# Kernel optimization log

Hardware: AMD Instinct MI355X
Metric: run time of the kernel (lower is better)

Reference implementation:

```python
import jax, jax.numpy as jnp
import numpy as np
from jax import lax

N = 14
K = 512
NUM_CLASSES = 10
TAO = 0.5 / (N * N)
BETA = 2.0


def make_t_p(n=N, tao=TAO, beta=BETA):
    # t_p[i, j, a, b] = tao * max(1 - beta * (|a-i| + |b-j|) / n, -1)
    idx = jnp.arange(n, dtype=jnp.float32)
    d = (jnp.abs(idx[:, None, None, None] - idx[None, None, :, None])
         + jnp.abs(idx[None, :, None, None] - idx[None, None, None, :]))
    return (tao * jnp.maximum(1.0 - beta * d / n, -1.0)).astype(jnp.float32)


def masked_output(x, t_p):
    # Vectorized equivalent of computeMaskedOutput: global spatial argmax per
    # (batch, channel) selects a template, then masked = relu(x * template).
    B, H, W, C = x.shape
    flat_idx = jnp.argmax(x.reshape(B, H * W, C), axis=1)      # [B, C]
    pi, pj = flat_idx // W, flat_idx % W
    tpl = t_p[pi, pj]                                          # [B, C, H, W]
    tpl = jnp.transpose(tpl, (0, 2, 3, 1))                     # [B, H, W, C]
    masked = jax.nn.relu(x * tpl)
    return masked, x, tpl


def compute_loss(x, pos_templates, act_sums, cls_sums, gt):
    # Fused segment-sum form of the original nested python loops.
    classes = jnp.zeros(NUM_CLASSES, x.dtype).at[gt].add(1.0)  # bincount
    cls_new = cls_sums + classes
    means = jnp.mean(x, axis=(1, 2))                           # [B, C]
    onehot = jax.nn.one_hot(gt, NUM_CLASSES, dtype=x.dtype)    # [B, 10]
    act_new = act_sums + means.T @ onehot                      # [C, 10]
    # divide_no_nan
    fm = jnp.where(cls_new[None, :] == 0, 0.0,
                   act_new / jnp.where(cls_new[None, :] == 0, 1.0, cls_new[None, :]))
    fclass = jnp.argmax(fm, axis=1)                            # [C]
    match = fclass[None, :] == gt[:, None]                     # [B, C]
    pt = jax.nn.relu(pos_templates)
    # relu(t_n) == 0 since t_n is strictly negative
    loss = jnp.where(match[:, None, None, :], pt, 0.0)
    return loss, act_new, cls_new


def forward(inputs, gt, conv_w, conv_b, dense_w, dense_b,
            activation_sums_1, activation_sums_2, class_sums_1, class_sums_2):
    t_p = make_t_p()
    raw_map = inputs  # base_model treated as identity on its feature map
    x1, X1_relu, pos_t1 = masked_output(raw_map, t_p)
    x3 = jax.nn.relu(lax.conv_general_dilated(
        x1, conv_w, window_strides=(1, 1), padding='SAME',
        dimension_numbers=('NHWC', 'HWIO', 'NHWC')) + conv_b)
    x2, X2_relu, pos_t2 = masked_output(x3, t_p)
    pooled = lax.reduce_window(x2, -jnp.inf, lax.max,
                               (1, 2, 2, 1), (1, 2, 2, 1), 'VALID')
    flat = pooled.reshape(pooled.shape[0], -1)
    probs = jax.nn.softmax(flat @ dense_w + dense_b, axis=-1)
    loss1, as1, cs1 = compute_loss(x1, pos_t1, activation_sums_1, class_sums_1, gt)
    loss2, as2, cs2 = compute_loss(x2, pos_t2, activation_sums_2, class_sums_2, gt)
    return probs, x1, x2, loss1, loss2, raw_map, pos_t1


def setup_inputs() -> dict:
    key = jax.random.key(0)
    ks = jax.random.split(key, 4)
    B = 128
    inputs = jax.random.uniform(ks[0], (B, N, N, K), dtype=jnp.float32)
    gt = jax.random.randint(ks[1], (B,), 0, NUM_CLASSES)
    conv_w = jax.random.normal(ks[2], (3, 3, K, K), dtype=jnp.float32) * 0.02
    conv_b = jnp.zeros((K,), jnp.float32)
    D = (N // 2) * (N // 2) * K  # 25088
    dense_w = jax.random.normal(ks[3], (D, NUM_CLASSES), dtype=jnp.float32) * 0.02
    dense_b = jnp.zeros((NUM_CLASSES,), jnp.float32)
    return {
        'inputs': inputs, 'gt': gt,
        'conv_w': conv_w, 'conv_b': conv_b,
        'dense_w': dense_w, 'dense_b': dense_b,
        'activation_sums_1': jnp.zeros((K, NUM_CLASSES), jnp.float32),
        'activation_sums_2': jnp.zeros((K, NUM_CLASSES), jnp.float32),
        'class_sums_1': jnp.zeros((NUM_CLASSES,), jnp.float32),
        'class_sums_2': jnp.zeros((NUM_CLASSES,), jnp.float32),
    }


def reference(inputs, gt, conv_w, conv_b, dense_w, dense_b,
              activation_sums_1, activation_sums_2, class_sums_1, class_sums_2):
    return forward(inputs, gt, conv_w, conv_b, dense_w, dense_b,
                   activation_sums_1, activation_sums_2,
                   class_sums_1, class_sums_2)
```

## Files before the change

kernel.cpp:

```cpp
#include <hip/hip_runtime.h>
#include <hip/hip_bf16.h>
#include <stdint.h>

#define TAO_F (0.5f/196.0f)

typedef short s16x8 __attribute__((ext_vector_type(8)));
typedef float f32x4 __attribute__((ext_vector_type(4)));
typedef __attribute__((address_space(1))) const unsigned int u32_g;
typedef __attribute__((address_space(3))) unsigned int u32_l;

__device__ __forceinline__ void async_ld16(const void* g, void* l) {
  __builtin_amdgcn_global_load_lds((u32_g*)g, (u32_l*)l, 16, 0, 0);
}

__global__ void k_prep_w(const float* __restrict__ w, __hip_bfloat16* __restrict__ wT) {
  __shared__ float tile[64][65];
  int bid = blockIdx.x;
  int r = bid / 64; int rem = bid - r * 64;
  int cib = (rem >> 3) * 64, cob = (rem & 7) * 64;
  int tid = threadIdx.x;
  int col = tid & 63, rw = tid >> 6;
#pragma unroll
  for (int p = 0; p < 16; ++p) {
    int row = p * 4 + rw;
    tile[row][col] = w[(size_t)(r * 512 + cib + row) * 512 + cob + col];
  }
  __syncthreads();
#pragma unroll
  for (int p = 0; p < 16; ++p) {
    int row = p * 4 + rw;
    wT[(size_t)(r * 512 + cob + row) * 512 + cib + col] = __float2bfloat16(tile[col][row]);
  }
}

__global__ void k_fuse1(const float* __restrict__ in, const int* __restrict__ gt,
                        float* __restrict__ o_raw, float* __restrict__ o_x1,
                        float* __restrict__ o_t1, __hip_bfloat16* __restrict__ x1p,
                        float* __restrict__ act1, int* __restrict__ idx1) {
  int t = blockIdx.x * 256 + threadIdx.x;
  int b = t >> 9, c = t & 511;
  const float* ip = in + (size_t)b * 196 * 512 + c;
  float* rp = o_raw + (size_t)b * 196 * 512 + c;
  float best = -1e30f; int bi = 0;
  for (int s = 0; s < 196; ++s) {
    float v = ip[(size_t)s * 512];
    rp[(size_t)s * 512] = v;
    if (v > best) { best = v; bi = s; }
  }
  idx1[t] = bi;
  int pi = bi / 14, pj = bi - pi * 14;
  float* ox = o_x1 + (size_t)b * 196 * 512 + c;
  float* ot = o_t1 + (size_t)b * 196 * 512 + c;
  __hip_bfloat16* xp = x1p + ((size_t)(b * 16 + 1) * 16 + 1) * 512 + c;
  float sum = 0.f;
  for (int i = 0; i < 14; ++i) {
    int di = (i > pi) ? (i - pi) : (pi - i);
    for (int j = 0; j < 14; ++j) {
      int d = di + ((j > pj) ? (j - pj) : (pj - j));
      float tpl = TAO_F * fmaxf(1.0f - (float)d / 7.0f, -1.0f);
      float x = ip[(size_t)(i * 14 + j) * 512];
      float m = fmaxf(x * tpl, 0.0f);
      ox[(size_t)(i * 14 + j) * 512] = m;
      ot[(size_t)(i * 14 + j) * 512] = tpl;
      xp[(size_t)(i * 16 + j) * 512] = __float2bfloat16(m);
      sum += m;
    }
  }
  atomicAdd(&act1[c * 10 + gt[b]], sum * (1.0f / 196.0f));
}

__global__ __launch_bounds__(256, 3) void k_gemm(const __hip_bfloat16* __restrict__ x1p,
                                                 const __hip_bfloat16* __restrict__ wT,
                                                 const float* __restrict__ conv_b,
                                                 float* __restrict__ x3) {
  int bid = blockIdx.x;
  int nt4 = bid & 3; int mt196 = bid >> 2;
  int m0 = mt196 * 128, co0 = nt4 * 128;
  int tid = threadIdx.x;
  int lane = tid & 63;

  __shared__ short As[128 * 64];
  __shared__ short Bs[128 * 64];

  int srow = tid >> 3;
  int sslot = tid & 7;
  int sx = ((sslot ^ (srow & 7)) * 8);

  int baseA[4];
#pragma unroll
  for (int p = 0; p < 4; ++p) {
    int m = m0 + p * 32 + srow;
    int b = m / 196; int s = m - b * 196; int i = s / 14; int j = s - i * 14;
    baseA[p] = ((b * 16 + i + 1) * 16 + (j + 1)) * 512;
  }
  int baseB[4];
#pragma unroll
  for (int p = 0; p < 4; ++p) baseB[p] = (co0 + p * 32 + srow) * 512;

  f32x4 acc[4][4] = {};

  int m_off = (tid >> 7) * 64;
  int n_off = ((tid >> 6) & 1) * 64;
  int q = lane >> 4;
  int l16 = lane & 15;

  for (int r = 0; r < 9; ++r) {
    int offr = ((r / 3) * 16 + (r % 3) - 17) * 512;
    int wbase = r * 512 * 512;
    for (int cb = 0; cb < 8; ++cb) {
      int ko = cb * 64;
      __syncthreads();
#pragma unroll
      for (int p = 0; p < 4; ++p) {
        async_ld16(x1p + (baseA[p] + offr + ko + sx),
                   &As[(p * 32 + srow) * 64 + sslot * 8]);
        async_ld16(wT + (wbase + baseB[p] + ko + sx),
                   &Bs[(p * 32 + srow) * 64 + sslot * 8]);
      }
      __syncthreads();
#pragma unroll
      for (int kk = 0; kk < 2; ++kk) {
        s16x8 af[4], bf[4];
#pragma unroll
        for (int tt = 0; tt < 4; ++tt) {
          int rowa = m_off + tt * 16 + l16;
          int sa = (kk * 4 + q) ^ (rowa & 7);
          af[tt] = *(const s16x8*)&As[rowa * 64 + sa * 8];
          int rowb = n_off + tt * 16 + l16;
          int sb = (kk * 4 + q) ^ (rowb & 7);
          bf[tt] = *(const s16x8*)&Bs[rowb * 64 + sb * 8];
        }
#pragma unroll
        for (int mt = 0; mt < 4; ++mt)
#pragma unroll
          for (int nt = 0; nt < 4; ++nt)
            acc[mt][nt] = __builtin_amdgcn_mfma_f32_16x16x32_bf16(af[mt], bf[nt], acc[mt][nt], 0, 0, 0);
      }
    }
  }
#pragma unroll
  for (int nt = 0; nt < 4; ++nt) {
    int col = co0 + n_off + nt * 16 + l16;
    float bias = conv_b[col];
#pragma unroll
    for (int mt = 0; mt < 4; ++mt) {
      int mrow = m0 + m_off + mt * 16 + q * 4;
#pragma unroll
      for (int rg = 0; rg < 4; ++rg) {
        float v = acc[mt][nt][rg] + bias;
        x3[(size_t)(mrow + rg) * 512 + col] = fmaxf(v, 0.0f);
      }
    }
  }
}

__global__ void k_fuse2(const float* __restrict__ x3, const int* __restrict__ gt,
                        const float* __restrict__ dw, float* __restrict__ o_x2,
                        float* __restrict__ act2, float* __restrict__ logits,
                        int* __restrict__ idx2) {
  int t = blockIdx.x * 256 + threadIdx.x;
  int b = t >> 9, c = t & 511;
  const float* ip = x3 + (size_t)b * 196 * 512 + c;
  float best = -1e30f; int bi = 0;
  for (int s = 0; s < 196; ++s) {
    float v = ip[(size_t)s * 512];
    if (v > best) { best = v; bi = s; }
  }
  idx2[t] = bi;
  int pi = bi / 14, pj = bi - pi * 14;
  float* ox = o_x2 + (size_t)b * 196 * 512 + c;
  float sum = 0.f;
  float a[10] = {0.f,0.f,0.f,0.f,0.f,0.f,0.f,0.f,0.f,0.f};
  for (int ii = 0; ii < 7; ++ii) {
    float rv[2][14];
#pragma unroll
    for (int r2 = 0; r2 < 2; ++r2) {
      int i = 2 * ii + r2;
      int di = (i > pi) ? (i - pi) : (pi - i);
#pragma unroll
      for (int j = 0; j < 14; ++j) {
        int d = di + ((j > pj) ? (j - pj) : (pj - j));
        float tpl = TAO_F * fmaxf(1.0f - (float)d / 7.0f, -1.0f);
        float x = ip[(size_t)(i * 14 + j) * 512];
        float m = fmaxf(x * tpl, 0.0f);
        ox[(size_t)(i * 14 + j) * 512] = m;
        sum += m;
        rv[r2][j] = m;
      }
    }
#pragma unroll
    for (int jj = 0; jj < 7; ++jj) {
      float pm = fmaxf(fmaxf(rv[0][2 * jj], rv[0][2 * jj + 1]),
                       fmaxf(rv[1][2 * jj], rv[1][2 * jj + 1]));
      const float* wr = dw + ((size_t)((ii * 7 + jj) * 512 + c)) * 10;
#pragma unroll
      for (int t2 = 0; t2 < 10; ++t2) a[t2] += pm * wr[t2];
    }
  }
  atomicAdd(&act2[c * 10 + gt[b]], sum * (1.0f / 196.0f));
  __shared__ float red[10];
  if (threadIdx.x < 10) red[threadIdx.x] = 0.f;
  __syncthreads();
  int lane = threadIdx.x & 63;
#pragma unroll
  for (int t2 = 0; t2 < 10; ++t2) {
    float v = a[t2];
    for (int off = 32; off > 0; off >>= 1) v += __shfl_down(v, off);
    if (lane == 0) atomicAdd(&red[t2], v);
  }
  __syncthreads();
  if (threadIdx.x < 10) atomicAdd(&logits[b * 10 + threadIdx.x], red[threadIdx.x]);
}

__global__ void k_stats(const float* __restrict__ act1, const float* __restrict__ act2,
                        const float* __restrict__ as1, const float* __restrict__ as2,
                        const float* __restrict__ cs1, const float* __restrict__ cs2,
                        const int* __restrict__ gt, const float* __restrict__ logits,
                        const float* __restrict__ db, int* __restrict__ fc1,
                        int* __restrict__ fc2, float* __restrict__ o_probs) {
  __shared__ int scnt[10];
  int tid = threadIdx.x;
  if (tid < 10) scnt[tid] = 0;
  __syncthreads();
  if (tid < 128) atomicAdd(&scnt[gt[tid]], 1);
  __syncthreads();
  int c = tid;
  float best1 = -1e30f, best2 = -1e30f; int b1 = 0, b2 = 0;
#pragma unroll
  for (int g = 0; g < 10; ++g) {
    float cnt = (float)scnt[g];
    float cn1 = cs1[g] + cnt;
    float cn2 = cs2[g] + cnt;
    float a1 = act1[c * 10 + g] + as1[c * 10 + g];
    float a2 = act2[c * 10 + g] + as2[c * 10 + g];
    float f1 = (cn1 == 0.f) ? 0.f : a1 / cn1;
    float f2 = (cn2 == 0.f) ? 0.f : a2 / cn2;
    if (f1 > best1) { best1 = f1; b1 = g; }
    if (f2 > best2) { best2 = f2; b2 = g; }
  }
  fc1[c] = b1; fc2[c] = b2;
  if (tid < 128) {
    float l[10]; float m = -1e30f;
#pragma unroll
    for (int t2 = 0; t2 < 10; ++t2) { l[t2] = logits[tid * 10 + t2] + db[t2]; m = fmaxf(m, l[t2]); }
    float s = 0.f;
#pragma unroll
    for (int t2 = 0; t2 < 10; ++t2) { l[t2] = expf(l[t2] - m); s += l[t2]; }
    float inv = 1.0f / s;
#pragma unroll
    for (int t2 = 0; t2 < 10; ++t2) o_probs[tid * 10 + t2] = l[t2] * inv;
  }
}

__global__ void k_loss(const int* __restrict__ idx1, const int* __restrict__ idx2,
                       const int* __restrict__ fc1, const int* __restrict__ fc2,
                       const int* __restrict__ gt, float* __restrict__ o1, float* __restrict__ o2) {
  int t = blockIdx.x * 256 + threadIdx.x;
  int b = t >> 9, c = t & 511;
  int g = gt[b];
  bool m1 = (fc1[c] == g), m2 = (fc2[c] == g);
  int i1 = idx1[t], i2 = idx2[t];
  int p1i = i1 / 14, p1j = i1 - p1i * 14;
  int p2i = i2 / 14, p2j = i2 - p2i * 14;
  float* w1 = o1 + (size_t)b * 196 * 512 + c;
  float* w2 = o2 + (size_t)b * 196 * 512 + c;
  for (int i = 0; i < 14; ++i) {
    int d1i = (i > p1i) ? (i - p1i) : (p1i - i);
    int d2i = (i > p2i) ? (i - p2i) : (p2i - i);
    for (int j = 0; j < 14; ++j) {
      int d1 = d1i + ((j > p1j) ? (j - p1j) : (p1j - j));
      int d2 = d2i + ((j > p2j) ? (j - p2j) : (p2j - j));
      float r1 = TAO_F * fmaxf(1.0f - (float)d1 / 7.0f, 0.0f);
      float r2 = TAO_F * fmaxf(1.0f - (float)d2 / 7.0f, 0.0f);
      w1[(size_t)(i * 14 + j) * 512] = m1 ? r1 : 0.0f;
      w2[(size_t)(i * 14 + j) * 512] = m2 ? r2 : 0.0f;
    }
  }
}

extern "C" void kernel_launch(void* const* d_in, const int* in_sizes, int n_in,
                              void* d_out, int out_size, void* d_ws, size_t ws_size,
                              hipStream_t stream) {
  const float* inputs  = (const float*)d_in[0];
  const int*   gt      = (const int*)d_in[1];
  const float* conv_w  = (const float*)d_in[2];
  const float* conv_b  = (const float*)d_in[3];
  const float* dense_w = (const float*)d_in[4];
  const float* dense_b = (const float*)d_in[5];
  const float* as1     = (const float*)d_in[6];
  const float* as2     = (const float*)d_in[7];
  const float* cs1     = (const float*)d_in[8];
  const float* cs2     = (const float*)d_in[9];

  float* out = (float*)d_out;
  const size_t S = 12845056;
  float* o_probs = out;
  float* o_x1  = out + 1280;
  float* o_x2  = o_x1 + S;
  float* o_l1  = o_x2 + S;
  float* o_l2  = o_l1 + S;
  float* o_raw = o_l2 + S;
  float* o_t1  = o_raw + S;

  uint8_t* w8 = (uint8_t*)d_ws;
  __hip_bfloat16* x1p = (__hip_bfloat16*)w8;
  float* x3  = (float*)(w8 + 33554432);
  __hip_bfloat16* wT = (__hip_bfloat16*)(w8 + 84934656);
  int*   idx1 = (int*)(w8 + 89653248);
  int*   idx2 = (int*)(w8 + 89915392);
  float* act1 = (float*)(w8 + 90177536);
  float* act2 = (float*)(w8 + 90198016);
  float* logits = (float*)(w8 + 90218496);
  int*   fc1  = (int*)(w8 + 90223616);
  int*   fc2  = (int*)(w8 + 90225664);

  hipMemsetAsync(x1p, 0, 33554432, stream);
  hipMemsetAsync(act1, 0, 46080, stream);

  k_prep_w<<<576, 256, 0, stream>>>(conv_w, wT);
  k_fuse1 <<<256, 256, 0, stream>>>(inputs, gt, o_raw, o_x1, o_t1, x1p, act1, idx1);
  k_gemm  <<<784, 256, 0, stream>>>(x1p, wT, conv_b, x3);
  k_fuse2 <<<256, 256, 0, stream>>>(x3, gt, dense_w, o_x2, act2, logits, idx2);
  k_stats <<<1, 512, 0, stream>>>(act1, act2, as1, as2, cs1, cs2, gt, logits, dense_b,
                                  fc1, fc2, o_probs);
  k_loss  <<<256, 256, 0, stream>>>(idx1, idx2, fc1, fc2, gt, o_l1, o_l2);
}
```

Baseline: 623.9 us.

## Parallelize elementwise kernels over spatial positions with float4 and block reductions

The memory-bound fuse1, fuse2 and loss kernels previously used one thread per (batch, channel) and only 256 blocks. They now spread each batch's spatial positions across threads, use float4 vector loads and stores, and do the argmax and sum reductions in shared memory. This gives 2048 or 1792 blocks instead of 256. Weight prep and fuse1 are merged into one launch, and fuse2 keeps its tile in LDS for the pooling and dense stage. The cost is extra syncthreads and reduction overhead in every block, and the argmax tie-breaking now depends on an explicit lower-index rule.

```diff
diff --git a/kernel.cpp b/kernel.cpp
--- a/kernel.cpp
+++ b/kernel.cpp
@@ -13,60 +13,124 @@
   __builtin_amdgcn_global_load_lds((u32_g*)g, (u32_l*)l, 16, 0, 0);
 }
 
-__global__ void k_prep_w(const float* __restrict__ w, __hip_bfloat16* __restrict__ wT) {
-  __shared__ float tile[64][65];
-  int bid = blockIdx.x;
-  int r = bid / 64; int rem = bid - r * 64;
-  int cib = (rem >> 3) * 64, cob = (rem & 7) * 64;
-  int tid = threadIdx.x;
-  int col = tid & 63, rw = tid >> 6;
-#pragma unroll
-  for (int p = 0; p < 16; ++p) {
-    int row = p * 4 + rw;
-    tile[row][col] = w[(size_t)(r * 512 + cib + row) * 512 + cob + col];
-  }
-  __syncthreads();
-#pragma unroll
-  for (int p = 0; p < 16; ++p) {
-    int row = p * 4 + rw;
-    wT[(size_t)(r * 512 + cob + row) * 512 + cib + col] = __float2bfloat16(tile[col][row]);
-  }
-}
-
-__global__ void k_fuse1(const float* __restrict__ in, const int* __restrict__ gt,
-                        float* __restrict__ o_raw, float* __restrict__ o_x1,
-                        float* __restrict__ o_t1, __hip_bfloat16* __restrict__ x1p,
-                        float* __restrict__ act1, int* __restrict__ idx1) {
-  int t = blockIdx.x * 256 + threadIdx.x;
-  int b = t >> 9, c = t & 511;
-  const float* ip = in + (size_t)b * 196 * 512 + c;
-  float* rp = o_raw + (size_t)b * 196 * 512 + c;
-  float best = -1e30f; int bi = 0;
-  for (int s = 0; s < 196; ++s) {
-    float v = ip[(size_t)s * 512];
-    rp[(size_t)s * 512] = v;
-    if (v > best) { best = v; bi = s; }
-  }
-  idx1[t] = bi;
-  int pi = bi / 14, pj = bi - pi * 14;
-  float* ox = o_x1 + (size_t)b * 196 * 512 + c;
-  float* ot = o_t1 + (size_t)b * 196 * 512 + c;
-  __hip_bfloat16* xp = x1p + ((size_t)(b * 16 + 1) * 16 + 1) * 512 + c;
-  float sum = 0.f;
-  for (int i = 0; i < 14; ++i) {
-    int di = (i > pi) ? (i - pi) : (pi - i);
-    for (int j = 0; j < 14; ++j) {
-      int d = di + ((j > pj) ? (j - pj) : (pj - j));
-      float tpl = TAO_F * fmaxf(1.0f - (float)d / 7.0f, -1.0f);
-      float x = ip[(size_t)(i * 14 + j) * 512];
-      float m = fmaxf(x * tpl, 0.0f);
-      ox[(size_t)(i * 14 + j) * 512] = m;
-      ot[(size_t)(i * 14 + j) * 512] = tpl;
-      xp[(size_t)(i * 16 + j) * 512] = __float2bfloat16(m);
-      sum += m;
-    }
-  }
-  atomicAdd(&act1[c * 10 + gt[b]], sum * (1.0f / 196.0f));
+__device__ __forceinline__ void fuse1_body(
+    int bid, const float* __restrict__ in, const int* __restrict__ gt,
+    float* __restrict__ o_raw, float* __restrict__ o_x1, float* __restrict__ o_t1,
+    __hip_bfloat16* __restrict__ x1p, float* __restrict__ act1,
+    int* __restrict__ idx1, uint8_t* smem) {
+  int b = bid >> 4, cg = bid & 15;
+  int t = threadIdx.x;
+  int c4 = t & 7, sp = t >> 3;
+  int c0 = cg * 32 + c4 * 4;
+  int cq = c0 >> 2;
+  float (*rv)[8][4] = (float(*)[8][4])smem;
+  int   (*ri)[8][4] = (int(*)[8][4])(smem + 4096);
+
+  const float4* ip = (const float4*)in + (size_t)b * 196 * 128;
+  float4* rp = (float4*)o_raw + (size_t)b * 196 * 128;
+
+  float bv[4] = {-1e30f, -1e30f, -1e30f, -1e30f};
+  int bix[4] = {0, 0, 0, 0};
+  for (int s = sp; s < 196; s += 32) {
+    float4 v = ip[s * 128 + cq];
+    rp[s * 128 + cq] = v;
+    float vv[4] = {v.x, v.y, v.z, v.w};
+#pragma unroll
+    for (int k = 0; k < 4; ++k)
+      if (vv[k] > bv[k]) { bv[k] = vv[k]; bix[k] = s; }
+  }
+#pragma unroll
+  for (int k = 0; k < 4; ++k) { rv[sp][c4][k] = bv[k]; ri[sp][c4][k] = bix[k]; }
+  __syncthreads();
+  for (int st = 16; st >= 1; st >>= 1) {
+    if (sp < st) {
+#pragma unroll
+      for (int k = 0; k < 4; ++k) {
+        float v1 = rv[sp][c4][k], v2 = rv[sp + st][c4][k];
+        int i1 = ri[sp][c4][k], i2 = ri[sp + st][c4][k];
+        if (v2 > v1 || (v2 == v1 && i2 < i1)) { rv[sp][c4][k] = v2; ri[sp][c4][k] = i2; }
+      }
+    }
+    __syncthreads();
+  }
+  int pi[4], pj[4];
+#pragma unroll
+  for (int k = 0; k < 4; ++k) {
+    int id = ri[0][c4][k];
+    pi[k] = id / 14; pj[k] = id - pi[k] * 14;
+  }
+  if (sp == 0)
+    *(int4*)&idx1[b * 512 + c0] = make_int4(ri[0][c4][0], ri[0][c4][1], ri[0][c4][2], ri[0][c4][3]);
+  __syncthreads();
+
+  float4* xo = (float4*)o_x1 + (size_t)b * 196 * 128;
+  float4* to = (float4*)o_t1 + (size_t)b * 196 * 128;
+  float sm[4] = {0.f, 0.f, 0.f, 0.f};
+  for (int s = sp; s < 196; s += 32) {
+    int i = s / 14, j = s - i * 14;
+    float4 x = ip[s * 128 + cq];
+    float xx[4] = {x.x, x.y, x.z, x.w};
+    float tp[4], mm[4];
+#pragma unroll
+    for (int k = 0; k < 4; ++k) {
+      int di = i - pi[k]; di = di < 0 ? -di : di;
+      int dj = j - pj[k]; dj = dj < 0 ? -dj : dj;
+      tp[k] = TAO_F * fmaxf(1.0f - (float)(di + dj) * (1.0f / 7.0f), -1.0f);
+      mm[k] = fmaxf(xx[k] * tp[k], 0.0f);
+      sm[k] += mm[k];
+    }
+    xo[s * 128 + cq] = make_float4(mm[0], mm[1], mm[2], mm[3]);
+    to[s * 128 + cq] = make_float4(tp[0], tp[1], tp[2], tp[3]);
+    union { ushort4 u4; __hip_bfloat16 h[4]; } cv;
+#pragma unroll
+    for (int k = 0; k < 4; ++k) cv.h[k] = __float2bfloat16(mm[k]);
+    *(ushort4*)&x1p[((size_t)(b * 16 + i + 1) * 16 + (j + 1)) * 512 + c0] = cv.u4;
+  }
+#pragma unroll
+  for (int k = 0; k < 4; ++k) rv[sp][c4][k] = sm[k];
+  __syncthreads();
+  for (int st = 16; st >= 1; st >>= 1) {
+    if (sp < st) {
+#pragma unroll
+      for (int k = 0; k < 4; ++k) rv[sp][c4][k] += rv[sp + st][c4][k];
+    }
+    __syncthreads();
+  }
+  if (sp == 0) {
+    int g = gt[b];
+#pragma unroll
+    for (int k = 0; k < 4; ++k)
+      atomicAdd(&act1[(c0 + k) * 10 + g], rv[0][c4][k] * (1.0f / 196.0f));
+  }
+}
+
+__global__ __launch_bounds__(256) void k_pre(
+    const float* __restrict__ w, __hip_bfloat16* __restrict__ wT,
+    const float* __restrict__ in, const int* __restrict__ gt,
+    float* __restrict__ o_raw, float* __restrict__ o_x1, float* __restrict__ o_t1,
+    __hip_bfloat16* __restrict__ x1p, float* __restrict__ act1, int* __restrict__ idx1) {
+  __shared__ uint8_t smem[16640];
+  if (blockIdx.x < 576) {
+    float (*tile)[65] = (float(*)[65])smem;
+    int bid = blockIdx.x;
+    int r = bid / 64; int rem = bid - r * 64;
+    int cib = (rem >> 3) * 64, cob = (rem & 7) * 64;
+    int tid = threadIdx.x;
+    int col = tid & 63, rw = tid >> 6;
+#pragma unroll
+    for (int p = 0; p < 16; ++p) {
+      int row = p * 4 + rw;
+      tile[row][col] = w[(size_t)(r * 512 + cib + row) * 512 + cob + col];
+    }
+    __syncthreads();
+#pragma unroll
+    for (int p = 0; p < 16; ++p) {
+      int row = p * 4 + rw;
+      wT[(size_t)(r * 512 + cob + row) * 512 + cib + col] = __float2bfloat16(tile[col][row]);
+    }
+  } else {
+    fuse1_body(blockIdx.x - 576, in, gt, o_raw, o_x1, o_t1, x1p, act1, idx1, smem);
+  }
 }
 
 __global__ __launch_bounds__(256, 3) void k_gemm(const __hip_bfloat16* __restrict__ x1p,
@@ -154,54 +218,106 @@
   }
 }
 
-__global__ void k_fuse2(const float* __restrict__ x3, const int* __restrict__ gt,
-                        const float* __restrict__ dw, float* __restrict__ o_x2,
-                        float* __restrict__ act2, float* __restrict__ logits,
-                        int* __restrict__ idx2) {
-  int t = blockIdx.x * 256 + threadIdx.x;
-  int b = t >> 9, c = t & 511;
-  const float* ip = x3 + (size_t)b * 196 * 512 + c;
-  float best = -1e30f; int bi = 0;
-  for (int s = 0; s < 196; ++s) {
-    float v = ip[(size_t)s * 512];
-    if (v > best) { best = v; bi = s; }
-  }
-  idx2[t] = bi;
-  int pi = bi / 14, pj = bi - pi * 14;
-  float* ox = o_x2 + (size_t)b * 196 * 512 + c;
-  float sum = 0.f;
+__global__ __launch_bounds__(256) void k_fuse2(
+    const float* __restrict__ x3, const int* __restrict__ gt,
+    const float* __restrict__ dw, float* __restrict__ o_x2,
+    float* __restrict__ act2, float* __restrict__ logits, int* __restrict__ idx2) {
+  __shared__ float4 vals[196][8];
+  __shared__ float rv[32][8][4];
+  __shared__ int   ri[32][8][4];
+  __shared__ float red[10];
+  int bid = blockIdx.x; int b = bid >> 4, cg = bid & 15;
+  int t = threadIdx.x, c4 = t & 7, sp = t >> 3;
+  int c0 = cg * 32 + c4 * 4, cq = c0 >> 2;
+  const float4* ip = (const float4*)x3 + (size_t)b * 196 * 128;
+
+  float bv[4] = {-1e30f, -1e30f, -1e30f, -1e30f};
+  int bix[4] = {0, 0, 0, 0};
+  for (int s = sp; s < 196; s += 32) {
+    float4 v = ip[s * 128 + cq];
+    vals[s][c4] = v;
+    float vv[4] = {v.x, v.y, v.z, v.w};
+#pragma unroll
+    for (int k = 0; k < 4; ++k)
+      if (vv[k] > bv[k]) { bv[k] = vv[k]; bix[k] = s; }
+  }
+#pragma unroll
+  for (int k = 0; k < 4; ++k) { rv[sp][c4][k] = bv[k]; ri[sp][c4][k] = bix[k]; }
+  __syncthreads();
+  for (int st = 16; st >= 1; st >>= 1) {
+    if (sp < st) {
+#pragma unroll
+      for (int k = 0; k < 4; ++k) {
+        float v1 = rv[sp][c4][k], v2 = rv[sp + st][c4][k];
+        int i1 = ri[sp][c4][k], i2 = ri[sp + st][c4][k];
+        if (v2 > v1 || (v2 == v1 && i2 < i1)) { rv[sp][c4][k] = v2; ri[sp][c4][k] = i2; }
+      }
+    }
+    __syncthreads();
+  }
+  int pi[4], pj[4];
+#pragma unroll
+  for (int k = 0; k < 4; ++k) {
+    int id = ri[0][c4][k];
+    pi[k] = id / 14; pj[k] = id - pi[k] * 14;
+  }
+  if (sp == 0)
+    *(int4*)&idx2[b * 512 + c0] = make_int4(ri[0][c4][0], ri[0][c4][1], ri[0][c4][2], ri[0][c4][3]);
+  if (t < 10) red[t] = 0.f;
+  __syncthreads();
+
+  float4* xo = (float4*)o_x2 + (size_t)b * 196 * 128;
+  float sm[4] = {0.f, 0.f, 0.f, 0.f};
+  for (int s = sp; s < 196; s += 32) {
+    int i = s / 14, j = s - i * 14;
+    float4 x = vals[s][c4];
+    float xx[4] = {x.x, x.y, x.z, x.w};
+    float mm[4];
+#pragma unroll
+    for (int k = 0; k < 4; ++k) {
+      int di = i - pi[k]; di = di < 0 ? -di : di;
+      int dj = j - pj[k]; dj = dj < 0 ? -dj : dj;
+      float tp = TAO_F * fmaxf(1.0f - (float)(di + dj) * (1.0f / 7.0f), -1.0f);
+      mm[k] = fmaxf(xx[k] * tp, 0.0f);
+      sm[k] += mm[k];
+    }
+    float4 m4 = make_float4(mm[0], mm[1], mm[2], mm[3]);
+    xo[s * 128 + cq] = m4;
+    vals[s][c4] = m4;
+  }
+#pragma unroll
+  for (int k = 0; k < 4; ++k) rv[sp][c4][k] = sm[k];
+  __syncthreads();
+  for (int st = 16; st >= 1; st >>= 1) {
+    if (sp < st) {
+#pragma unroll
+      for (int k = 0; k < 4; ++k) rv[sp][c4][k] += rv[sp + st][c4][k];
+    }
+    __syncthreads();
+  }
+  if (sp == 0) {
+    int g = gt[b];
+#pragma unroll
+    for (int k = 0; k < 4; ++k)
+      atomicAdd(&act2[(c0 + k) * 10 + g], rv[0][c4][k] * (1.0f / 196.0f));
+  }
+
   float a[10] = {0.f,0.f,0.f,0.f,0.f,0.f,0.f,0.f,0.f,0.f};
-  for (int ii = 0; ii < 7; ++ii) {
-    float rv[2][14];
-#pragma unroll
-    for (int r2 = 0; r2 < 2; ++r2) {
-      int i = 2 * ii + r2;
-      int di = (i > pi) ? (i - pi) : (pi - i);
-#pragma unroll
-      for (int j = 0; j < 14; ++j) {
-        int d = di + ((j > pj) ? (j - pj) : (pj - j));
-        float tpl = TAO_F * fmaxf(1.0f - (float)d / 7.0f, -1.0f);
-        float x = ip[(size_t)(i * 14 + j) * 512];
-        float m = fmaxf(x * tpl, 0.0f);
-        ox[(size_t)(i * 14 + j) * 512] = m;
-        sum += m;
-        rv[r2][j] = m;
-      }
-    }
-#pragma unroll
-    for (int jj = 0; jj < 7; ++jj) {
-      float pm = fmaxf(fmaxf(rv[0][2 * jj], rv[0][2 * jj + 1]),
-                       fmaxf(rv[1][2 * jj], rv[1][2 * jj + 1]));
-      const float* wr = dw + ((size_t)((ii * 7 + jj) * 512 + c)) * 10;
-#pragma unroll
-      for (int t2 = 0; t2 < 10; ++t2) a[t2] += pm * wr[t2];
-    }
-  }
-  atomicAdd(&act2[c * 10 + gt[b]], sum * (1.0f / 196.0f));
-  __shared__ float red[10];
-  if (threadIdx.x < 10) red[threadIdx.x] = 0.f;
-  __syncthreads();
-  int lane = threadIdx.x & 63;
+  for (int pp = sp; pp < 49; pp += 32) {
+    int ii = pp / 7, jj = pp - ii * 7;
+    int s00 = (2 * ii) * 14 + 2 * jj;
+    float4 v00 = vals[s00][c4], v01 = vals[s00 + 1][c4];
+    float4 v10 = vals[s00 + 14][c4], v11 = vals[s00 + 15][c4];
+    float pmx = fmaxf(fmaxf(v00.x, v01.x), fmaxf(v10.x, v11.x));
+    float pmy = fmaxf(fmaxf(v00.y, v01.y), fmaxf(v10.y, v11.y));
+    float pmz = fmaxf(fmaxf(v00.z, v01.z), fmaxf(v10.z, v11.z));
+    float pmw = fmaxf(fmaxf(v00.w, v01.w), fmaxf(v10.w, v11.w));
+    const float* wr = dw + ((size_t)((ii * 7 + jj) * 512 + c0)) * 10;
+#pragma unroll
+    for (int t2 = 0; t2 < 10; ++t2)
+      a[t2] += pmx * wr[t2] + pmy * wr[10 + t2] + pmz * wr[20 + t2] + pmw * wr[30 + t2];
+  }
+  int lane = t & 63;
 #pragma unroll
   for (int t2 = 0; t2 < 10; ++t2) {
     float v = a[t2];
@@ -209,7 +325,7 @@
     if (lane == 0) atomicAdd(&red[t2], v);
   }
   __syncthreads();
-  if (threadIdx.x < 10) atomicAdd(&logits[b * 10 + threadIdx.x], red[threadIdx.x]);
+  if (t < 10) atomicAdd(&logits[b * 10 + t], red[t]);
 }
 
 __global__ void k_stats(const float* __restrict__ act1, const float* __restrict__ act2,
@@ -252,29 +368,48 @@
   }
 }
 
-__global__ void k_loss(const int* __restrict__ idx1, const int* __restrict__ idx2,
-                       const int* __restrict__ fc1, const int* __restrict__ fc2,
-                       const int* __restrict__ gt, float* __restrict__ o1, float* __restrict__ o2) {
-  int t = blockIdx.x * 256 + threadIdx.x;
-  int b = t >> 9, c = t & 511;
+__global__ __launch_bounds__(256) void k_loss(
+    const int* __restrict__ idx1, const int* __restrict__ idx2,
+    const int* __restrict__ fc1, const int* __restrict__ fc2,
+    const int* __restrict__ gt, float* __restrict__ o1, float* __restrict__ o2) {
+  int bid = blockIdx.x;
+  int b = bid / 14, i = bid - b * 14;
+  int t = threadIdx.x;
+  int cgp = t & 127, jh = t >> 7;
+  int c0 = cgp * 4;
   int g = gt[b];
-  bool m1 = (fc1[c] == g), m2 = (fc2[c] == g);
-  int i1 = idx1[t], i2 = idx2[t];
-  int p1i = i1 / 14, p1j = i1 - p1i * 14;
-  int p2i = i2 / 14, p2j = i2 - p2i * 14;
-  float* w1 = o1 + (size_t)b * 196 * 512 + c;
-  float* w2 = o2 + (size_t)b * 196 * 512 + c;
-  for (int i = 0; i < 14; ++i) {
-    int d1i = (i > p1i) ? (i - p1i) : (p1i - i);
-    int d2i = (i > p2i) ? (i - p2i) : (p2i - i);
-    for (int j = 0; j < 14; ++j) {
-      int d1 = d1i + ((j > p1j) ? (j - p1j) : (p1j - j));
-      int d2 = d2i + ((j > p2j) ? (j - p2j) : (p2j - j));
-      float r1 = TAO_F * fmaxf(1.0f - (float)d1 / 7.0f, 0.0f);
-      float r2 = TAO_F * fmaxf(1.0f - (float)d2 / 7.0f, 0.0f);
-      w1[(size_t)(i * 14 + j) * 512] = m1 ? r1 : 0.0f;
-      w2[(size_t)(i * 14 + j) * 512] = m2 ? r2 : 0.0f;
-    }
+  int4 i1 = *(const int4*)&idx1[b * 512 + c0];
+  int4 i2 = *(const int4*)&idx2[b * 512 + c0];
+  int4 f1 = *(const int4*)&fc1[c0];
+  int4 f2 = *(const int4*)&fc2[c0];
+  float ms1[4] = {f1.x == g ? 1.f : 0.f, f1.y == g ? 1.f : 0.f,
+                  f1.z == g ? 1.f : 0.f, f1.w == g ? 1.f : 0.f};
+  float ms2[4] = {f2.x == g ? 1.f : 0.f, f2.y == g ? 1.f : 0.f,
+                  f2.z == g ? 1.f : 0.f, f2.w == g ? 1.f : 0.f};
+  int p1i[4], p1j[4], p2i[4], p2j[4];
+  int ia1[4] = {i1.x, i1.y, i1.z, i1.w};
+  int ia2[4] = {i2.x, i2.y, i2.z, i2.w};
+#pragma unroll
+  for (int k = 0; k < 4; ++k) {
+    p1i[k] = ia1[k] / 14; p1j[k] = ia1[k] - p1i[k] * 14;
+    p2i[k] = ia2[k] / 14; p2j[k] = ia2[k] - p2i[k] * 14;
+  }
+  float4* w1 = (float4*)o1 + ((size_t)b * 196 + i * 14) * 128 + (c0 >> 2);
+  float4* w2 = (float4*)o2 + ((size_t)b * 196 + i * 14) * 128 + (c0 >> 2);
+  for (int jj = 0; jj < 7; ++jj) {
+    int j = jh * 7 + jj;
+    float r1[4], r2[4];
+#pragma unroll
+    for (int k = 0; k < 4; ++k) {
+      int d1i = i - p1i[k]; d1i = d1i < 0 ? -d1i : d1i;
+      int d1j = j - p1j[k]; d1j = d1j < 0 ? -d1j : d1j;
+      int d2i = i - p2i[k]; d2i = d2i < 0 ? -d2i : d2i;
+      int d2j = j - p2j[k]; d2j = d2j < 0 ? -d2j : d2j;
+      r1[k] = ms1[k] * (TAO_F * fmaxf(1.0f - (float)(d1i + d1j) * (1.0f / 7.0f), 0.0f));
+      r2[k] = ms2[k] * (TAO_F * fmaxf(1.0f - (float)(d2i + d2j) * (1.0f / 7.0f), 0.0f));
+    }
+    w1[(size_t)j * 128] = make_float4(r1[0], r1[1], r1[2], r1[3]);
+    w2[(size_t)j * 128] = make_float4(r2[0], r2[1], r2[2], r2[3]);
   }
 }
 
@@ -317,11 +452,11 @@
   hipMemsetAsync(x1p, 0, 33554432, stream);
   hipMemsetAsync(act1, 0, 46080, stream);
 
-  k_prep_w<<<576, 256, 0, stream>>>(conv_w, wT);
-  k_fuse1 <<<256, 256, 0, stream>>>(inputs, gt, o_raw, o_x1, o_t1, x1p, act1, idx1);
+  k_pre   <<<576 + 2048, 256, 0, stream>>>(conv_w, wT, inputs, gt, o_raw, o_x1, o_t1,
+                                           x1p, act1, idx1);
   k_gemm  <<<784, 256, 0, stream>>>(x1p, wT, conv_b, x3);
-  k_fuse2 <<<256, 256, 0, stream>>>(x3, gt, dense_w, o_x2, act2, logits, idx2);
+  k_fuse2 <<<2048, 256, 0, stream>>>(x3, gt, dense_w, o_x2, act2, logits, idx2);
   k_stats <<<1, 512, 0, stream>>>(act1, act2, as1, as2, cs1, cs2, gt, logits, dense_b,
                                   fc1, fc2, o_probs);
-  k_loss  <<<256, 256, 0, stream>>>(idx1, idx2, fc1, fc2, gt, o_l1, o_l2);
-}
+  k_loss  <<<1792, 256, 0, stream>>>(idx1, idx2, fc1, fc2, gt, o_l1, o_l2);
+}
```

Result: faster. 594.5 us (-4.7%).
